# Optimization experiments

Measured on AMD Instinct MI355X. Metric: run time of the kernel, lower is better.

## Reference

```python
import jax, jax.numpy as jnp
import numpy as np

L, H, C, V, T_BLK = 12, 12, 768, 50257, 1024
D = C // H  # head dim = 64


def _layernorm(x, g, b, eps=1e-5):
    m = jnp.mean(x, axis=-1, keepdims=True)
    v = jnp.mean(jnp.square(x - m), axis=-1, keepdims=True)
    return (x - m) * jax.lax.rsqrt(v + eps) * g + b


def setup_inputs() -> dict:
    key = jax.random.key(0)
    ks = jax.random.split(key, 8)
    B, T = 8, 1024
    s = 0.02
    sp = 0.02 / np.sqrt(2 * L)  # c_proj special init
    return {
        "idx": jax.random.randint(ks[0], (B, T), 0, V, dtype=jnp.int32),
        "wte": jax.random.normal(ks[1], (V, C), jnp.float32) * s,
        "wpe": jax.random.normal(ks[2], (T_BLK, C), jnp.float32) * s,
        "ln1_g": jnp.ones((L, C), jnp.float32),
        "ln1_b": jnp.zeros((L, C), jnp.float32),
        "w_qkv": jax.random.normal(ks[3], (L, C, 3 * C), jnp.float32) * s,
        "b_qkv": jnp.zeros((L, 3 * C), jnp.float32),
        "w_ao": jax.random.normal(ks[4], (L, C, C), jnp.float32) * sp,
        "b_ao": jnp.zeros((L, C), jnp.float32),
        "ln2_g": jnp.ones((L, C), jnp.float32),
        "ln2_b": jnp.zeros((L, C), jnp.float32),
        "w_fc": jax.random.normal(ks[5], (L, C, 4 * C), jnp.float32) * s,
        "b_fc": jnp.zeros((L, 4 * C), jnp.float32),
        "w_mo": jax.random.normal(ks[6], (L, 4 * C, C), jnp.float32) * sp,
        "b_mo": jnp.zeros((L, C), jnp.float32),
        "lnf_g": jnp.ones((C,), jnp.float32),
        "lnf_b": jnp.zeros((C,), jnp.float32),
    }


def reference(idx, wte, wpe, ln1_g, ln1_b, w_qkv, b_qkv, w_ao, b_ao,
              ln2_g, ln2_b, w_fc, b_fc, w_mo, b_mo, lnf_g, lnf_b):
    B, T = idx.shape
    scale = 1.0 / np.sqrt(D)
    causal = jnp.tril(jnp.ones((T, T), dtype=bool))  # [T,T]

    x = wte[idx] + wpe[:T]  # [B,T,C]

    def block(x, p):
        g1, b1, wq, bq, wo, bo, g2, b2_, wf, bf, w2, b2m = p
        h = _layernorm(x, g1, b1)
        qkv = h @ wq + bq  # [B,T,3C]
        q, k, v = jnp.split(qkv, 3, axis=-1)
        q = q.reshape(B, T, H, D)
        k = k.reshape(B, T, H, D)
        v = v.reshape(B, T, H, D)
        att = jnp.einsum('bqhd,bkhd->bhqk', q, k) * scale
        att = jnp.where(causal, att, -jnp.inf)
        att = jax.nn.softmax(att, axis=-1)
        y = jnp.einsum('bhqk,bkhd->bqhd', att, v).reshape(B, T, C)
        x = x + y @ wo + bo
        h2 = _layernorm(x, g2, b2_)
        x = x + jax.nn.gelu(h2 @ wf + bf, approximate=False) @ w2 + b2m
        return x, None

    params = (ln1_g, ln1_b, w_qkv, b_qkv, w_ao, b_ao,
              ln2_g, ln2_b, w_fc, b_fc, w_mo, b_mo)
    x, _ = jax.lax.scan(block, x, params)

    x = _layernorm(x, lnf_g, lnf_b)
    # inference path: logits only for last position, lm_head tied to wte
    logits = x[:, -1:, :] @ wte.T  # [B,1,V]
    return logits
```

## Files before the change

### kernel.cpp

```cpp
#include <hip/hip_runtime.h>

#define B_ 8
#define T_ 1024
#define C_ 768
#define H_ 12
#define L_ 12
#define V_ 50257

typedef __bf16 bf16_t;
typedef __bf16 bf16x8 __attribute__((ext_vector_type(8)));
typedef __bf16 bf16x4 __attribute__((ext_vector_type(4)));
typedef float f32x4 __attribute__((ext_vector_type(4)));

__device__ __forceinline__ unsigned short f2bf(float f) {
  bf16_t h = (bf16_t)f;
  return __builtin_bit_cast(unsigned short, h);
}

__device__ __forceinline__ unsigned short bfbits(bf16_t h) {
  return __builtin_bit_cast(unsigned short, h);
}

template<int CTRL>
__device__ __forceinline__ float dppf(float x) {
  return __builtin_bit_cast(float, __builtin_amdgcn_update_dpp(
      0, __builtin_bit_cast(int, x), CTRL, 0xF, 0xF, true));
}
__device__ __forceinline__ float red16_max(float x) {
  x = fmaxf(x, dppf<0xB1>(x));
  x = fmaxf(x, dppf<0x4E>(x));
  x = fmaxf(x, dppf<0x124>(x));
  x = fmaxf(x, dppf<0x128>(x));
  return x;
}
__device__ __forceinline__ float red16_sum(float x) {
  x += dppf<0xB1>(x);
  x += dppf<0x4E>(x);
  x += dppf<0x124>(x);
  x += dppf<0x128>(x);
  return x;
}

__global__ __launch_bounds__(192) void embed_kernel(
    const int* __restrict__ idx, const float* __restrict__ wte,
    const float* __restrict__ wpe, float* __restrict__ xf)
{
  const int bt = blockIdx.x;
  const int t = bt & (T_ - 1);
  const int tok = idx[bt];
  const int c4 = threadIdx.x << 2;
  float4 a = *(const float4*)(wte + (size_t)tok * C_ + c4);
  float4 p = *(const float4*)(wpe + (size_t)t * C_ + c4);
  float4 r; r.x = a.x + p.x; r.y = a.y + p.y; r.z = a.z + p.z; r.w = a.w + p.w;
  *(float4*)(xf + (size_t)bt * C_ + c4) = r;
}

template<bool LAST>
__global__ __launch_bounds__(256) void ln_kernel(
    const float* __restrict__ x, const float* __restrict__ gw,
    const float* __restrict__ bw, unsigned short* __restrict__ obf,
    float* __restrict__ of)
{
  __shared__ float red[8];
  const size_t row = LAST ? ((size_t)blockIdx.x * T_ + (T_ - 1)) : (size_t)blockIdx.x;
  const float* xr = x + row * C_;
  const int t = threadIdx.x;
  float v0 = xr[t], v1 = xr[t + 256], v2 = xr[t + 512];
  float s = v0 + v1 + v2;
  #pragma unroll
  for (int off = 32; off; off >>= 1) s += __shfl_xor(s, off);
  if ((t & 63) == 0) red[t >> 6] = s;
  __syncthreads();
  const float mean = (red[0] + red[1] + red[2] + red[3]) * (1.0f / C_);
  const float d0 = v0 - mean, d1 = v1 - mean, d2 = v2 - mean;
  float ss = d0 * d0 + d1 * d1 + d2 * d2;
  #pragma unroll
  for (int off = 32; off; off >>= 1) ss += __shfl_xor(ss, off);
  if ((t & 63) == 0) red[4 + (t >> 6)] = ss;
  __syncthreads();
  const float var = (red[4] + red[5] + red[6] + red[7]) * (1.0f / C_);
  const float rs = rsqrtf(var + 1e-5f);
  float o0 = d0 * rs * gw[t] + bw[t];
  float o1 = d1 * rs * gw[t + 256] + bw[t + 256];
  float o2 = d2 * rs * gw[t + 512] + bw[t + 512];
  if (LAST) {
    float* orow = of + (size_t)blockIdx.x * C_;
    orow[t] = o0; orow[t + 256] = o1; orow[t + 512] = o2;
  } else {
    unsigned short* orow = obf + row * C_;
    orow[t] = f2bf(o0); orow[t + 256] = f2bf(o1); orow[t + 512] = f2bf(o2);
  }
}

__global__ __launch_bounds__(256) void cvtw4_kernel(
    const float* __restrict__ wq, const float* __restrict__ wa,
    const float* __restrict__ wf, const float* __restrict__ wm,
    unsigned short* __restrict__ out)
{
  __shared__ float tile[32][33];
  const int i = blockIdx.x;
  const float* W; unsigned short* Wt; int K, N, tix;
  if (i < 1728)      { W = wq; Wt = out;                 K = C_;     N = 3 * C_; tix = i; }
  else if (i < 2304) { W = wa; Wt = out + 3 * C_ * C_;   K = C_;     N = C_;     tix = i - 1728; }
  else if (i < 4608) { W = wf; Wt = out + 4 * C_ * C_;   K = C_;     N = 4 * C_; tix = i - 2304; }
  else               { W = wm; Wt = out + 8 * C_ * C_;   K = 4 * C_; N = C_;     tix = i - 4608; }
  const int ntx = N >> 5;
  const int kb = (tix / ntx) << 5, nb = (tix % ntx) << 5;
  const int t = threadIdx.x;
  {
    const int k = t >> 3, n4 = (t & 7) << 2;
    float4 v = *(const float4*)(W + (size_t)(kb + k) * N + nb + n4);
    tile[k][n4] = v.x; tile[k][n4 + 1] = v.y; tile[k][n4 + 2] = v.z; tile[k][n4 + 3] = v.w;
  }
  __syncthreads();
  {
    const int n = t >> 3, k4 = (t & 7) << 2;
    ushort4 o;
    o.x = f2bf(tile[k4][n]);     o.y = f2bf(tile[k4 + 1][n]);
    o.z = f2bf(tile[k4 + 2][n]); o.w = f2bf(tile[k4 + 3][n]);
    *(ushort4*)(Wt + (size_t)(nb + n) * K + kb + k4) = o;
  }
}

template<int EPI>
__global__ __launch_bounds__(256, 2) void gemm_bt(
    const unsigned short* __restrict__ A, const unsigned short* __restrict__ Bt,
    const float* __restrict__ bias, float* __restrict__ Cf,
    unsigned short* __restrict__ Cb, int M, int N, int K, int nx)
{
  __shared__ unsigned short As[2][128 * 64];
  __shared__ unsigned short Bs[2][128 * 64];
  const int tid = threadIdx.x;
  const int lane = tid & 63;
  const int w = tid >> 6;
  const int wr = w >> 1, wc = w & 1;
  const int l15 = lane & 15, l4 = lane >> 4;
  const int swz = lane & 7;

  const int nwg = gridDim.x;
  int wg = blockIdx.x;
  wg = (wg & 7) * (nwg >> 3) + (wg >> 3);
  const int mblk = wg / nx;
  const int nblk = wg - mblk * nx;
  const int m0 = mblk * 128, n0 = nblk * 128;

  f32x4 acc[4][4] = {};

  const int srow = lane >> 3;
  const int schunk = (lane & 7) ^ srow;
  const unsigned short* aSrc = A + (size_t)(m0 + w * 32 + srow) * K + schunk * 8;
  const unsigned short* bSrc = Bt + (size_t)(n0 + w * 32 + srow) * K + schunk * 8;
  const int ldsRowBase = (w * 32) * 64;

  auto stage = [&](int kt, int p) {
    const int k0 = kt << 6;
    #pragma unroll
    for (int j = 0; j < 4; ++j)
      __builtin_amdgcn_global_load_lds(
          (const __attribute__((address_space(1))) unsigned int*)(aSrc + (size_t)j * 8 * K + k0),
          (__attribute__((address_space(3))) unsigned int*)(&As[p][ldsRowBase + j * 8 * 64]), 16, 0, 0);
    #pragma unroll
    for (int j = 0; j < 4; ++j)
      __builtin_amdgcn_global_load_lds(
          (const __attribute__((address_space(1))) unsigned int*)(bSrc + (size_t)j * 8 * K + k0),
          (__attribute__((address_space(3))) unsigned int*)(&Bs[p][ldsRowBase + j * 8 * 64]), 16, 0, 0);
  };

  auto compute = [&](int p) {
    const unsigned short* aw = &As[p][(wr * 64) * 64];
    const unsigned short* bw2 = &Bs[p][(wc * 64) * 64];
    #pragma unroll
    for (int ks = 0; ks < 2; ++ks) {
      bf16x8 af[4], bf[4];
      #pragma unroll
      for (int mf = 0; mf < 4; ++mf)
        af[mf] = *(const bf16x8*)(aw + (mf * 16 + l15) * 64 + (((ks << 2) | l4) ^ swz) * 8);
      #pragma unroll
      for (int nf = 0; nf < 4; ++nf)
        bf[nf] = *(const bf16x8*)(bw2 + (nf * 16 + l15) * 64 + (((ks << 2) | l4) ^ swz) * 8);
      __builtin_amdgcn_s_setprio(1);
      #pragma unroll
      for (int mf = 0; mf < 4; ++mf)
        #pragma unroll
        for (int nf = 0; nf < 4; ++nf)
          acc[mf][nf] = __builtin_amdgcn_mfma_f32_16x16x32_bf16(af[mf], bf[nf], acc[mf][nf], 0, 0, 0);
      __builtin_amdgcn_s_setprio(0);
    }
  };

  const int nk = K >> 6;
  stage(0, 0);
  for (int kt = 0; kt < nk - 1; ++kt) {
    const int p = kt & 1;
    stage(kt + 1, p ^ 1);
    asm volatile("s_waitcnt vmcnt(8)" ::: "memory");
    __builtin_amdgcn_s_barrier();
    compute(p);
    __builtin_amdgcn_s_barrier();
  }
  asm volatile("s_waitcnt vmcnt(0)" ::: "memory");
  __builtin_amdgcn_s_barrier();
  compute((nk - 1) & 1);

  #pragma unroll
  for (int mf = 0; mf < 4; ++mf) {
    #pragma unroll
    for (int nf = 0; nf < 4; ++nf) {
      const int col = n0 + wc * 64 + nf * 16 + l15;
      const float bv = bias[col];
      int hh = 0, dd = 0;
      unsigned short* qkvo = nullptr;
      if constexpr (EPI == 3) {
        const int which = col / C_;
        const int rem = col - which * C_;
        hh = rem >> 6; dd = rem & 63;
        qkvo = Cb + (size_t)which * ((size_t)B_ * H_ * T_ * 64);
      }
      #pragma unroll
      for (int i = 0; i < 4; ++i) {
        const int row = m0 + wr * 64 + mf * 16 + l4 * 4 + i;
        float v = acc[mf][nf][i] + bv;
        if constexpr (EPI == 0) {
          Cf[(size_t)row * N + col] = v;
        } else if constexpr (EPI == 1) {
          Cf[(size_t)row * N + col] += v;
        } else if constexpr (EPI == 2) {
          float g = 0.5f * v * (1.0f + erff(v * 0.70710678118f));
          Cb[(size_t)row * N + col] = f2bf(g);
        } else {
          const int bb = row >> 10, tt = row & (T_ - 1);
          qkvo[(((size_t)bb * H_ + hh) * T_ + tt) * 64 + dd] = f2bf(v);
        }
      }
    }
  }
}

__global__ __launch_bounds__(256) void attn_kernel(
    const unsigned short* __restrict__ Qb, const unsigned short* __restrict__ Kb,
    const unsigned short* __restrict__ Vb, unsigned short* __restrict__ y)
{
  const int pb = blockIdx.x / 96;
  const int bh = blockIdx.x % 96;
  const int h = bh % H_;
  const int b = bh / H_;
  const int tid = threadIdx.x, lane = tid & 63, w = tid >> 6;
  const int l15 = lane & 15, l4 = lane >> 4;

  const int qw = (w < 2) ? (pb * 64 + w * 32) : ((15 - pb) * 64 + (w - 2) * 32);
  const int NT = (17 - pb) >> 1;

  __shared__ unsigned short Ks[128 * 64];
  __shared__ unsigned short Vt[64 * 136];
  __shared__ unsigned short Pb[4][32 * 74];

  const unsigned short* qp = Qb + ((size_t)bh * T_ + qw) * 64;
  bf16x8 qf[2][2];
  #pragma unroll
  for (int mf = 0; mf < 2; ++mf)
    #pragma unroll
    for (int ks = 0; ks < 2; ++ks)
      qf[mf][ks] = *(const bf16x8*)(qp + (mf * 16 + l15) * 64 + ks * 32 + l4 * 8);

  f32x4 o[2][4] = {};
  float mrow[2][4], lrow[2][4];
  #pragma unroll
  for (int mf = 0; mf < 2; ++mf)
    #pragma unroll
    for (int i = 0; i < 4; ++i) { mrow[mf][i] = -1e30f; lrow[mf][i] = 0.0f; }

  const unsigned short* kb0 = Kb + (size_t)bh * T_ * 64;
  const unsigned short* vb0 = Vb + (size_t)bh * T_ * 64;
  const int ck = w;
  const int skey = lane;
  const int sw = (skey & 7);

  bf16x8 kr0, kr1, kr2, kr3, vr0, vr1, vr2, vr3;
  {
    const unsigned short* kp = kb0 + (size_t)skey * 64;
    const unsigned short* vp = vb0 + (size_t)skey * 64;
    kr0 = *(const bf16x8*)(kp + ck * 8);
    kr1 = *(const bf16x8*)(kp + (ck + 4) * 8);
    kr2 = *(const bf16x8*)(kp + 64 * 64 + ck * 8);
    kr3 = *(const bf16x8*)(kp + 64 * 64 + (ck + 4) * 8);
    vr0 = *(const bf16x8*)(vp + ck * 8);
    vr1 = *(const bf16x8*)(vp + (ck + 4) * 8);
    vr2 = *(const bf16x8*)(vp + 64 * 64 + ck * 8);
    vr3 = *(const bf16x8*)(vp + 64 * 64 + (ck + 4) * 8);
  }

  for (int kt = 0; kt < NT; ++kt) {
    const int k0 = kt << 7;
    __syncthreads();
    *(bf16x8*)(Ks + skey * 64 + ((ck ^ sw) * 8)) = kr0;
    *(bf16x8*)(Ks + skey * 64 + (((ck + 4) ^ sw) * 8)) = kr1;
    *(bf16x8*)(Ks + (skey + 64) * 64 + ((ck ^ sw) * 8)) = kr2;
    *(bf16x8*)(Ks + (skey + 64) * 64 + (((ck + 4) ^ sw) * 8)) = kr3;
    #pragma unroll
    for (int j = 0; j < 8; ++j) {
      Vt[(ck * 8 + j) * 136 + skey]            = bfbits(vr0[j]);
      Vt[((ck + 4) * 8 + j) * 136 + skey]      = bfbits(vr1[j]);
      Vt[(ck * 8 + j) * 136 + skey + 64]       = bfbits(vr2[j]);
      Vt[((ck + 4) * 8 + j) * 136 + skey + 64] = bfbits(vr3[j]);
    }
    __syncthreads();
    if (kt + 1 < NT) {
      const int kn = (kt + 1) << 7;
      const unsigned short* kp = kb0 + (size_t)(kn + skey) * 64;
      const unsigned short* vp = vb0 + (size_t)(kn + skey) * 64;
      kr0 = *(const bf16x8*)(kp + ck * 8);
      kr1 = *(const bf16x8*)(kp + (ck + 4) * 8);
      kr2 = *(const bf16x8*)(kp + 64 * 64 + ck * 8);
      kr3 = *(const bf16x8*)(kp + 64 * 64 + (ck + 4) * 8);
      vr0 = *(const bf16x8*)(vp + ck * 8);
      vr1 = *(const bf16x8*)(vp + (ck + 4) * 8);
      vr2 = *(const bf16x8*)(vp + 64 * 64 + ck * 8);
      vr3 = *(const bf16x8*)(vp + 64 * 64 + (ck + 4) * 8);
    }

    #pragma unroll
    for (int h2 = 0; h2 < 2; ++h2) {
      const int kh0 = k0 + h2 * 64;
      if (kh0 > qw + 31) continue;

      f32x4 s[2][4] = {};
      __builtin_amdgcn_s_setprio(1);
      #pragma unroll
      for (int ks = 0; ks < 2; ++ks) {
        #pragma unroll
        for (int nfk = 0; nfk < 4; ++nfk) {
          const int key = h2 * 64 + nfk * 16 + l15;
          bf16x8 kf = *(const bf16x8*)(Ks + key * 64 + ((((ks << 2) | l4) ^ (l15 & 7)) * 8));
          #pragma unroll
          for (int mf = 0; mf < 2; ++mf)
            s[mf][nfk] = __builtin_amdgcn_mfma_f32_16x16x32_bf16(qf[mf][ks], kf, s[mf][nfk], 0, 0, 0);
        }
      }
      __builtin_amdgcn_s_setprio(0);

      #pragma unroll
      for (int mf = 0; mf < 2; ++mf) {
        const int qrow = qw + mf * 16 + l4 * 4;
        const bool fullt = (kh0 + 63) <= (qw + mf * 16);
        float alpha[4];
        float pvv[4][4];
        #pragma unroll
        for (int i = 0; i < 4; ++i) {
          const int q = qrow + i;
          float sv[4], tm = -1e30f;
          #pragma unroll
          for (int nfk = 0; nfk < 4; ++nfk) {
            float x = s[mf][nfk][i] * 0.125f;
            sv[nfk] = fullt ? x : ((kh0 + nfk * 16 + l15 <= q) ? x : -1e30f);
            tm = fmaxf(tm, sv[nfk]);
          }
          tm = red16_max(tm);
          const float mnew = fmaxf(mrow[mf][i], tm);
          alpha[i] = __expf(mrow[mf][i] - mnew);
          mrow[mf][i] = mnew;
          float rsum = 0.0f;
          #pragma unroll
          for (int nfk = 0; nfk < 4; ++nfk) {
            const float p = __expf(sv[nfk] - mnew);
            pvv[nfk][i] = p; rsum += p;
          }
          rsum = red16_sum(rsum);
          lrow[mf][i] = lrow[mf][i] * alpha[i] + rsum;
        }
        #pragma unroll
        for (int nf = 0; nf < 4; ++nf)
          #pragma unroll
          for (int i = 0; i < 4; ++i)
            o[mf][nf][i] *= alpha[i];
        #pragma unroll
        for (int nfk = 0; nfk < 4; ++nfk)
          #pragma unroll
          for (int i = 0; i < 4; ++i)
            Pb[w][(mf * 16 + l4 * 4 + i) * 74 + nfk * 16 + l15] = f2bf(pvv[nfk][i]);
      }

      bf16x8 pa[2][2];
      #pragma unroll
      for (int mf = 0; mf < 2; ++mf)
        #pragma unroll
        for (int k2 = 0; k2 < 2; ++k2)
          pa[mf][k2] = *(const bf16x8*)(Pb[w] + (mf * 16 + l15) * 74 + k2 * 32 + l4 * 8);
      __builtin_amdgcn_s_setprio(1);
      #pragma unroll
      for (int nf = 0; nf < 4; ++nf) {
        const int d = nf * 16 + l15;
        #pragma unroll
        for (int k2 = 0; k2 < 2; ++k2) {
          bf16x8 vf = *(const bf16x8*)(Vt + d * 136 + h2 * 64 + k2 * 32 + l4 * 8);
          #pragma unroll
          for (int mf = 0; mf < 2; ++mf)
            o[mf][nf] = __builtin_amdgcn_mfma_f32_16x16x32_bf16(pa[mf][k2], vf, o[mf][nf], 0, 0, 0);
        }
      }
      __builtin_amdgcn_s_setprio(0);
    }
  }

  #pragma unroll
  for (int mf = 0; mf < 2; ++mf) {
    #pragma unroll
    for (int i = 0; i < 4; ++i) {
      const float inv = 1.0f / lrow[mf][i];
      const int q = qw + mf * 16 + l4 * 4 + i;
      unsigned short* yr = y + (size_t)(b * T_ + q) * C_ + h * 64;
      #pragma unroll
      for (int nf = 0; nf < 4; ++nf)
        yr[nf * 16 + l15] = f2bf(o[mf][nf][i] * inv);
    }
  }
}

__global__ __launch_bounds__(256) void head_kernel(
    const float* __restrict__ lnf, const float* __restrict__ wte,
    float* __restrict__ out)
{
  __shared__ float xs[B_ * C_];
  for (int i = threadIdx.x; i < B_ * C_; i += 256) xs[i] = lnf[i];
  __syncthreads();
  const int w = threadIdx.x >> 6, lane = threadIdx.x & 63;
  const int v = blockIdx.x * 4 + w;
  if (v >= V_) return;
  const float* wv = wte + (size_t)v * C_ + lane * 12;
  float4 w0 = *(const float4*)(wv);
  float4 w1 = *(const float4*)(wv + 4);
  float4 w2 = *(const float4*)(wv + 8);
  float acc[B_];
  #pragma unroll
  for (int bb = 0; bb < B_; ++bb) {
    const float* xr = xs + bb * C_ + lane * 12;
    float4 x0 = *(const float4*)(xr);
    float4 x1 = *(const float4*)(xr + 4);
    float4 x2 = *(const float4*)(xr + 8);
    acc[bb] = w0.x * x0.x + w0.y * x0.y + w0.z * x0.z + w0.w * x0.w
            + w1.x * x1.x + w1.y * x1.y + w1.z * x1.z + w1.w * x1.w
            + w2.x * x2.x + w2.y * x2.y + w2.z * x2.z + w2.w * x2.w;
  }
  #pragma unroll
  for (int off = 32; off; off >>= 1) {
    #pragma unroll
    for (int bb = 0; bb < B_; ++bb)
      acc[bb] += __shfl_xor(acc[bb], off);
  }
  if (lane == 0) {
    #pragma unroll
    for (int bb = 0; bb < B_; ++bb)
      out[(size_t)bb * V_ + v] = acc[bb];
  }
}

extern "C" void kernel_launch(void* const* d_in, const int* in_sizes, int n_in,
                              void* d_out, int out_size, void* d_ws, size_t ws_size,
                              hipStream_t stream)
{
  (void)in_sizes; (void)n_in; (void)out_size; (void)ws_size;
  const int*   idx   = (const int*)d_in[0];
  const float* wte   = (const float*)d_in[1];
  const float* wpe   = (const float*)d_in[2];
  const float* ln1_g = (const float*)d_in[3];
  const float* ln1_b = (const float*)d_in[4];
  const float* w_qkv = (const float*)d_in[5];
  const float* b_qkv = (const float*)d_in[6];
  const float* w_ao  = (const float*)d_in[7];
  const float* b_ao  = (const float*)d_in[8];
  const float* ln2_g = (const float*)d_in[9];
  const float* ln2_b = (const float*)d_in[10];
  const float* w_fc  = (const float*)d_in[11];
  const float* b_fc  = (const float*)d_in[12];
  const float* w_mo  = (const float*)d_in[13];
  const float* b_mo  = (const float*)d_in[14];
  const float* lnf_g = (const float*)d_in[15];
  const float* lnf_b = (const float*)d_in[16];

  char* ws = (char*)d_ws;
  size_t off = 0;
  auto wsalloc = [&](size_t bytes) -> void* {
    void* p = ws + off;
    off += (bytes + 255) & ~(size_t)255;
    return p;
  };
  const size_t SZH = (size_t)B_ * H_ * T_ * 64;
  float* xf             = (float*)wsalloc((size_t)B_ * T_ * C_ * 4);
  unsigned short* qkv3  = (unsigned short*)wsalloc(3 * SZH * 2);
  unsigned short* a_in  = (unsigned short*)wsalloc((size_t)B_ * T_ * C_ * 2);
  unsigned short* act2  = (unsigned short*)wsalloc((size_t)B_ * T_ * 4 * C_ * 2);
  unsigned short* wbuf  = (unsigned short*)wsalloc((size_t)12 * C_ * C_ * 2);
  float* lnfb           = (float*)wsalloc((size_t)B_ * C_ * 4);

  const size_t OFF_AO = (size_t)3 * C_ * C_;
  const size_t OFF_FC = (size_t)4 * C_ * C_;
  const size_t OFF_MO = (size_t)8 * C_ * C_;
  const int MROWS = B_ * T_;

  embed_kernel<<<B_ * T_, 192, 0, stream>>>(idx, wte, wpe, xf);

  for (int l = 0; l < L_; ++l) {
    ln_kernel<false><<<B_ * T_, 256, 0, stream>>>(xf, ln1_g + l * C_, ln1_b + l * C_, a_in, nullptr);
    cvtw4_kernel<<<6912, 256, 0, stream>>>(
        w_qkv + (size_t)l * C_ * 3 * C_, w_ao + (size_t)l * C_ * C_,
        w_fc + (size_t)l * C_ * 4 * C_, w_mo + (size_t)l * 4 * C_ * C_, wbuf);
    gemm_bt<3><<<18 * 64, 256, 0, stream>>>(a_in, wbuf, b_qkv + l * 3 * C_, nullptr, qkv3, MROWS, 3 * C_, C_, 18);
    attn_kernel<<<8 * B_ * H_, 256, 0, stream>>>(qkv3, qkv3 + SZH, qkv3 + 2 * SZH, a_in);
    gemm_bt<1><<<6 * 64, 256, 0, stream>>>(a_in, wbuf + OFF_AO, b_ao + l * C_, xf, nullptr, MROWS, C_, C_, 6);
    ln_kernel<false><<<B_ * T_, 256, 0, stream>>>(xf, ln2_g + l * C_, ln2_b + l * C_, a_in, nullptr);
    gemm_bt<2><<<24 * 64, 256, 0, stream>>>(a_in, wbuf + OFF_FC, b_fc + l * 4 * C_, nullptr, act2, MROWS, 4 * C_, C_, 24);
    gemm_bt<1><<<6 * 64, 256, 0, stream>>>(act2, wbuf + OFF_MO, b_mo + l * C_, xf, nullptr, MROWS, C_, 4 * C_, 6);
  }

  ln_kernel<true><<<B_, 256, 0, stream>>>(xf, lnf_g, lnf_b, nullptr, lnfb);
  head_kernel<<<(V_ + 3) / 4, 256, 0, stream>>>(lnfb, wte, (float*)d_out);
}
```

Measured before the change: 3.742 ms.

## Replace GEMM with 8-wave 256x128 tile kernel and interleaved fragment loads

Swaps the 4-wave 128x128 GEMM for a 512-thread kernel computing 256x128 tiles. Each wave owns a 64x64 sub-tile, and the kernel splits the MFMA work into four quadrants separated by barriers, with LDS fragment loads interleaved between them. The aim is more operand reuse per loaded B tile and overlap of LDS reads with matrix math. In exchange, the grid is halved: the 768-wide GEMMs launch only 192 workgroups, which may underfill the device, and the added barriers cost synchronisation.

```diff
diff --git a/kernel.cpp b/kernel.cpp
--- a/kernel.cpp
+++ b/kernel.cpp
@@ -11,6 +11,9 @@
 typedef __bf16 bf16x8 __attribute__((ext_vector_type(8)));
 typedef __bf16 bf16x4 __attribute__((ext_vector_type(4)));
 typedef float f32x4 __attribute__((ext_vector_type(4)));
+
+#define AS1 __attribute__((address_space(1)))
+#define AS3 __attribute__((address_space(3)))
 
 __device__ __forceinline__ unsigned short f2bf(float f) {
   bf16_t h = (bf16_t)f;
@@ -123,84 +126,126 @@
 }
 
 template<int EPI>
-__global__ __launch_bounds__(256, 2) void gemm_bt(
+__global__ __launch_bounds__(512, 1) void gemm8(
     const unsigned short* __restrict__ A, const unsigned short* __restrict__ Bt,
     const float* __restrict__ bias, float* __restrict__ Cf,
     unsigned short* __restrict__ Cb, int M, int N, int K, int nx)
 {
-  __shared__ unsigned short As[2][128 * 64];
-  __shared__ unsigned short Bs[2][128 * 64];
+  __shared__ __align__(16) unsigned short As[2][2][128 * 64];
+  __shared__ __align__(16) unsigned short Bs[2][128 * 64];
   const int tid = threadIdx.x;
   const int lane = tid & 63;
   const int w = tid >> 6;
-  const int wr = w >> 1, wc = w & 1;
+  const int wr = w >> 1;
+  const int wc = w & 1;
   const int l15 = lane & 15, l4 = lane >> 4;
-  const int swz = lane & 7;
+  const int s7 = l15 & 7;
+  const int hA = wr >> 1;
+  const int rbase = (wr & 1) * 64;
 
   const int nwg = gridDim.x;
   int wg = blockIdx.x;
   wg = (wg & 7) * (nwg >> 3) + (wg >> 3);
   const int mblk = wg / nx;
   const int nblk = wg - mblk * nx;
-  const int m0 = mblk * 128, n0 = nblk * 128;
+  const int m0 = mblk * 256, n0 = nblk * 128;
 
   f32x4 acc[4][4] = {};
 
-  const int srow = lane >> 3;
-  const int schunk = (lane & 7) ^ srow;
-  const unsigned short* aSrc = A + (size_t)(m0 + w * 32 + srow) * K + schunk * 8;
-  const unsigned short* bSrc = Bt + (size_t)(n0 + w * 32 + srow) * K + schunk * 8;
-  const int ldsRowBase = (w * 32) * 64;
+  const int srow8 = lane >> 3;
+  const int schunk = (lane & 7) ^ srow8;
+  const unsigned short* aS00 = A  + (size_t)(m0 +       0 + w * 8 + srow8) * K + schunk * 8;
+  const unsigned short* aS01 = A  + (size_t)(m0 +      64 + w * 8 + srow8) * K + schunk * 8;
+  const unsigned short* aS10 = A  + (size_t)(m0 + 128 + 0 + w * 8 + srow8) * K + schunk * 8;
+  const unsigned short* aS11 = A  + (size_t)(m0 + 128 + 64 + w * 8 + srow8) * K + schunk * 8;
+  const unsigned short* bS0  = Bt + (size_t)(n0 +       0 + w * 8 + srow8) * K + schunk * 8;
+  const unsigned short* bS1  = Bt + (size_t)(n0 +      64 + w * 8 + srow8) * K + schunk * 8;
+  const int ldsw0 = (0 * 8 + w) * 512;
+  const int ldsw1 = (1 * 8 + w) * 512;
 
   auto stage = [&](int kt, int p) {
-    const int k0 = kt << 6;
-    #pragma unroll
-    for (int j = 0; j < 4; ++j)
-      __builtin_amdgcn_global_load_lds(
-          (const __attribute__((address_space(1))) unsigned int*)(aSrc + (size_t)j * 8 * K + k0),
-          (__attribute__((address_space(3))) unsigned int*)(&As[p][ldsRowBase + j * 8 * 64]), 16, 0, 0);
-    #pragma unroll
-    for (int j = 0; j < 4; ++j)
-      __builtin_amdgcn_global_load_lds(
-          (const __attribute__((address_space(1))) unsigned int*)(bSrc + (size_t)j * 8 * K + k0),
-          (__attribute__((address_space(3))) unsigned int*)(&Bs[p][ldsRowBase + j * 8 * 64]), 16, 0, 0);
-  };
-
-  auto compute = [&](int p) {
-    const unsigned short* aw = &As[p][(wr * 64) * 64];
-    const unsigned short* bw2 = &Bs[p][(wc * 64) * 64];
-    #pragma unroll
-    for (int ks = 0; ks < 2; ++ks) {
-      bf16x8 af[4], bf[4];
-      #pragma unroll
-      for (int mf = 0; mf < 4; ++mf)
-        af[mf] = *(const bf16x8*)(aw + (mf * 16 + l15) * 64 + (((ks << 2) | l4) ^ swz) * 8);
-      #pragma unroll
-      for (int nf = 0; nf < 4; ++nf)
-        bf[nf] = *(const bf16x8*)(bw2 + (nf * 16 + l15) * 64 + (((ks << 2) | l4) ^ swz) * 8);
-      __builtin_amdgcn_s_setprio(1);
-      #pragma unroll
-      for (int mf = 0; mf < 4; ++mf)
-        #pragma unroll
-        for (int nf = 0; nf < 4; ++nf)
-          acc[mf][nf] = __builtin_amdgcn_mfma_f32_16x16x32_bf16(af[mf], bf[nf], acc[mf][nf], 0, 0, 0);
-      __builtin_amdgcn_s_setprio(0);
-    }
+    const size_t k0 = (size_t)kt * 64;
+    __builtin_amdgcn_global_load_lds((const AS1 unsigned int*)(aS00 + k0), (AS3 unsigned int*)(&As[p][0][ldsw0]), 16, 0, 0);
+    __builtin_amdgcn_global_load_lds((const AS1 unsigned int*)(aS01 + k0), (AS3 unsigned int*)(&As[p][0][ldsw1]), 16, 0, 0);
+    __builtin_amdgcn_global_load_lds((const AS1 unsigned int*)(aS10 + k0), (AS3 unsigned int*)(&As[p][1][ldsw0]), 16, 0, 0);
+    __builtin_amdgcn_global_load_lds((const AS1 unsigned int*)(aS11 + k0), (AS3 unsigned int*)(&As[p][1][ldsw1]), 16, 0, 0);
+    __builtin_amdgcn_global_load_lds((const AS1 unsigned int*)(bS0  + k0), (AS3 unsigned int*)(&Bs[p][ldsw0]), 16, 0, 0);
+    __builtin_amdgcn_global_load_lds((const AS1 unsigned int*)(bS1  + k0), (AS3 unsigned int*)(&Bs[p][ldsw1]), 16, 0, 0);
   };
 
   const int nk = K >> 6;
   stage(0, 0);
-  for (int kt = 0; kt < nk - 1; ++kt) {
-    const int p = kt & 1;
-    stage(kt + 1, p ^ 1);
-    asm volatile("s_waitcnt vmcnt(8)" ::: "memory");
+
+  for (int t = 0; t < nk; ++t) {
+    const int p = t & 1;
+    bf16x8 af[4][2], bf[4][2];
+    auto rdA = [&](int mf, int ks) -> bf16x8 {
+      return *(const bf16x8*)(&As[p][hA][(rbase + mf * 16 + l15) * 64 + ((((ks << 2) | l4) ^ s7) << 3)]);
+    };
+    auto rdB = [&](int nf, int ks) -> bf16x8 {
+      return *(const bf16x8*)(&Bs[p][(wc * 64 + nf * 16 + l15) * 64 + ((((ks << 2) | l4) ^ s7) << 3)]);
+    };
+
+    if (t + 1 < nk) {
+      stage(t + 1, p ^ 1);
+      asm volatile("s_waitcnt vmcnt(6)" ::: "memory");
+    } else {
+      asm volatile("s_waitcnt vmcnt(0)" ::: "memory");
+    }
     __builtin_amdgcn_s_barrier();
-    compute(p);
+    #pragma unroll
+    for (int mf = 0; mf < 2; ++mf) { af[mf][0] = rdA(mf, 0); af[mf][1] = rdA(mf, 1); }
+    #pragma unroll
+    for (int nf = 0; nf < 2; ++nf) { bf[nf][0] = rdB(nf, 0); bf[nf][1] = rdB(nf, 1); }
+    __builtin_amdgcn_s_setprio(1);
+    #pragma unroll
+    for (int mf = 0; mf < 2; ++mf)
+      #pragma unroll
+      for (int nf = 0; nf < 2; ++nf)
+        #pragma unroll
+        for (int ks = 0; ks < 2; ++ks)
+          acc[mf][nf] = __builtin_amdgcn_mfma_f32_16x16x32_bf16(af[mf][ks], bf[nf][ks], acc[mf][nf], 0, 0, 0);
+    __builtin_amdgcn_s_setprio(0);
     __builtin_amdgcn_s_barrier();
-  }
-  asm volatile("s_waitcnt vmcnt(0)" ::: "memory");
-  __builtin_amdgcn_s_barrier();
-  compute((nk - 1) & 1);
+
+    #pragma unroll
+    for (int nf = 2; nf < 4; ++nf) { bf[nf][0] = rdB(nf, 0); bf[nf][1] = rdB(nf, 1); }
+    __builtin_amdgcn_s_barrier();
+    __builtin_amdgcn_s_setprio(1);
+    #pragma unroll
+    for (int mf = 0; mf < 2; ++mf)
+      #pragma unroll
+      for (int nf = 2; nf < 4; ++nf)
+        #pragma unroll
+        for (int ks = 0; ks < 2; ++ks)
+          acc[mf][nf] = __builtin_amdgcn_mfma_f32_16x16x32_bf16(af[mf][ks], bf[nf][ks], acc[mf][nf], 0, 0, 0);
+    __builtin_amdgcn_s_setprio(0);
+    __builtin_amdgcn_s_barrier();
+
+    #pragma unroll
+    for (int mf = 2; mf < 4; ++mf) { af[mf][0] = rdA(mf, 0); af[mf][1] = rdA(mf, 1); }
+    __builtin_amdgcn_s_barrier();
+    __builtin_amdgcn_s_setprio(1);
+    #pragma unroll
+    for (int mf = 2; mf < 4; ++mf)
+      #pragma unroll
+      for (int nf = 0; nf < 2; ++nf)
+        #pragma unroll
+        for (int ks = 0; ks < 2; ++ks)
+          acc[mf][nf] = __builtin_amdgcn_mfma_f32_16x16x32_bf16(af[mf][ks], bf[nf][ks], acc[mf][nf], 0, 0, 0);
+    __builtin_amdgcn_s_setprio(0);
+    __builtin_amdgcn_s_barrier();
+
+    __builtin_amdgcn_s_setprio(1);
+    #pragma unroll
+    for (int mf = 2; mf < 4; ++mf)
+      #pragma unroll
+      for (int nf = 2; nf < 4; ++nf)
+        #pragma unroll
+        for (int ks = 0; ks < 2; ++ks)
+          acc[mf][nf] = __builtin_amdgcn_mfma_f32_16x16x32_bf16(af[mf][ks], bf[nf][ks], acc[mf][nf], 0, 0, 0);
+    __builtin_amdgcn_s_setprio(0);
+  }
 
   #pragma unroll
   for (int mf = 0; mf < 4; ++mf) {
@@ -220,9 +265,7 @@
       for (int i = 0; i < 4; ++i) {
         const int row = m0 + wr * 64 + mf * 16 + l4 * 4 + i;
         float v = acc[mf][nf][i] + bv;
-        if constexpr (EPI == 0) {
-          Cf[(size_t)row * N + col] = v;
-        } else if constexpr (EPI == 1) {
+        if constexpr (EPI == 1) {
           Cf[(size_t)row * N + col] += v;
         } else if constexpr (EPI == 2) {
           float g = 0.5f * v * (1.0f + erff(v * 0.70710678118f));
@@ -503,12 +546,12 @@
     cvtw4_kernel<<<6912, 256, 0, stream>>>(
         w_qkv + (size_t)l * C_ * 3 * C_, w_ao + (size_t)l * C_ * C_,
         w_fc + (size_t)l * C_ * 4 * C_, w_mo + (size_t)l * 4 * C_ * C_, wbuf);
-    gemm_bt<3><<<18 * 64, 256, 0, stream>>>(a_in, wbuf, b_qkv + l * 3 * C_, nullptr, qkv3, MROWS, 3 * C_, C_, 18);
+    gemm8<3><<<32 * 18, 512, 0, stream>>>(a_in, wbuf, b_qkv + l * 3 * C_, nullptr, qkv3, MROWS, 3 * C_, C_, 18);
     attn_kernel<<<8 * B_ * H_, 256, 0, stream>>>(qkv3, qkv3 + SZH, qkv3 + 2 * SZH, a_in);
-    gemm_bt<1><<<6 * 64, 256, 0, stream>>>(a_in, wbuf + OFF_AO, b_ao + l * C_, xf, nullptr, MROWS, C_, C_, 6);
+    gemm8<1><<<32 * 6, 512, 0, stream>>>(a_in, wbuf + OFF_AO, b_ao + l * C_, xf, nullptr, MROWS, C_, C_, 6);
     ln_kernel<false><<<B_ * T_, 256, 0, stream>>>(xf, ln2_g + l * C_, ln2_b + l * C_, a_in, nullptr);
-    gemm_bt<2><<<24 * 64, 256, 0, stream>>>(a_in, wbuf + OFF_FC, b_fc + l * 4 * C_, nullptr, act2, MROWS, 4 * C_, C_, 24);
-    gemm_bt<1><<<6 * 64, 256, 0, stream>>>(act2, wbuf + OFF_MO, b_mo + l * C_, xf, nullptr, MROWS, C_, 4 * C_, 6);
+    gemm8<2><<<32 * 24, 512, 0, stream>>>(a_in, wbuf + OFF_FC, b_fc + l * 4 * C_, nullptr, act2, MROWS, 4 * C_, C_, 24);
+    gemm8<1><<<32 * 6, 512, 0, stream>>>(act2, wbuf + OFF_MO, b_mo + l * C_, xf, nullptr, MROWS, C_, 4 * C_, 6);
   }
 
   ln_kernel<true><<<B_, 256, 0, stream>>>(xf, lnf_g, lnf_b, nullptr, lnfb);
```

New measurement: 4.198 ms. 12.2% more time.

## Remap GEMM tiles per XCD and lazily rescale attention softmax max

Applied to the files above, without the earlier changes.

The GEMM block index mapping now gives each XCD a contiguous group of 8 M-blocks and walks N-blocks across the blocks of that XCD. The aim is for weight and activation tiles to be reused in each XCD's L2. The attention online softmax now rescales the accumulator and row sum only when some row's new max exceeds the stored max by more than 8, which is checked wave-wide with __any. This skips most exp and multiply rescale work, at the cost of probabilities that can grow up to e^8 before rescaling, which is safe in fp32 but may lose a little bf16 precision in P.

```diff
diff --git a/kernel.cpp b/kernel.cpp
--- a/kernel.cpp
+++ b/kernel.cpp
@@ -11,6 +11,9 @@
 typedef __bf16 bf16x8 __attribute__((ext_vector_type(8)));
 typedef __bf16 bf16x4 __attribute__((ext_vector_type(4)));
 typedef float f32x4 __attribute__((ext_vector_type(4)));
+
+#define AS1 __attribute__((address_space(1)))
+#define AS3 __attribute__((address_space(3)))
 
 __device__ __forceinline__ unsigned short f2bf(float f) {
   bf16_t h = (bf16_t)f;
@@ -128,6 +131,7 @@
     const float* __restrict__ bias, float* __restrict__ Cf,
     unsigned short* __restrict__ Cb, int M, int N, int K, int nx)
 {
+  (void)M; (void)nx;
   __shared__ unsigned short As[2][128 * 64];
   __shared__ unsigned short Bs[2][128 * 64];
   const int tid = threadIdx.x;
@@ -137,11 +141,11 @@
   const int l15 = lane & 15, l4 = lane >> 4;
   const int swz = lane & 7;
 
-  const int nwg = gridDim.x;
-  int wg = blockIdx.x;
-  wg = (wg & 7) * (nwg >> 3) + (wg >> 3);
-  const int mblk = wg / nx;
-  const int nblk = wg - mblk * nx;
+  const int bid = blockIdx.x;
+  const int xcd = bid & 7;
+  const int j = bid >> 3;
+  const int mblk = xcd * 8 + (j & 7);
+  const int nblk = j >> 3;
   const int m0 = mblk * 128, n0 = nblk * 128;
 
   f32x4 acc[4][4] = {};
@@ -155,15 +159,15 @@
   auto stage = [&](int kt, int p) {
     const int k0 = kt << 6;
     #pragma unroll
-    for (int j = 0; j < 4; ++j)
+    for (int jj = 0; jj < 4; ++jj)
       __builtin_amdgcn_global_load_lds(
-          (const __attribute__((address_space(1))) unsigned int*)(aSrc + (size_t)j * 8 * K + k0),
-          (__attribute__((address_space(3))) unsigned int*)(&As[p][ldsRowBase + j * 8 * 64]), 16, 0, 0);
-    #pragma unroll
-    for (int j = 0; j < 4; ++j)
+          (const AS1 unsigned int*)(aSrc + (size_t)jj * 8 * K + k0),
+          (AS3 unsigned int*)(&As[p][ldsRowBase + jj * 8 * 64]), 16, 0, 0);
+    #pragma unroll
+    for (int jj = 0; jj < 4; ++jj)
       __builtin_amdgcn_global_load_lds(
-          (const __attribute__((address_space(1))) unsigned int*)(bSrc + (size_t)j * 8 * K + k0),
-          (__attribute__((address_space(3))) unsigned int*)(&Bs[p][ldsRowBase + j * 8 * 64]), 16, 0, 0);
+          (const AS1 unsigned int*)(bSrc + (size_t)jj * 8 * K + k0),
+          (AS3 unsigned int*)(&Bs[p][ldsRowBase + jj * 8 * 64]), 16, 0, 0);
   };
 
   auto compute = [&](int p) {
@@ -220,9 +224,7 @@
       for (int i = 0; i < 4; ++i) {
         const int row = m0 + wr * 64 + mf * 16 + l4 * 4 + i;
         float v = acc[mf][nf][i] + bv;
-        if constexpr (EPI == 0) {
-          Cf[(size_t)row * N + col] = v;
-        } else if constexpr (EPI == 1) {
+        if constexpr (EPI == 1) {
           Cf[(size_t)row * N + col] += v;
         } else if constexpr (EPI == 2) {
           float g = 0.5f * v * (1.0f + erff(v * 0.70710678118f));
@@ -297,11 +299,11 @@
     *(bf16x8*)(Ks + (skey + 64) * 64 + ((ck ^ sw) * 8)) = kr2;
     *(bf16x8*)(Ks + (skey + 64) * 64 + (((ck + 4) ^ sw) * 8)) = kr3;
     #pragma unroll
-    for (int j = 0; j < 8; ++j) {
-      Vt[(ck * 8 + j) * 136 + skey]            = bfbits(vr0[j]);
-      Vt[((ck + 4) * 8 + j) * 136 + skey]      = bfbits(vr1[j]);
-      Vt[(ck * 8 + j) * 136 + skey + 64]       = bfbits(vr2[j]);
-      Vt[((ck + 4) * 8 + j) * 136 + skey + 64] = bfbits(vr3[j]);
+    for (int jj = 0; jj < 8; ++jj) {
+      Vt[(ck * 8 + jj) * 136 + skey]            = bfbits(vr0[jj]);
+      Vt[((ck + 4) * 8 + jj) * 136 + skey]      = bfbits(vr1[jj]);
+      Vt[(ck * 8 + jj) * 136 + skey + 64]       = bfbits(vr2[jj]);
+      Vt[((ck + 4) * 8 + jj) * 136 + skey + 64] = bfbits(vr3[jj]);
     }
     __syncthreads();
     if (kt + 1 < NT) {
@@ -342,36 +344,45 @@
       for (int mf = 0; mf < 2; ++mf) {
         const int qrow = qw + mf * 16 + l4 * 4;
         const bool fullt = (kh0 + 63) <= (qw + mf * 16);
-        float alpha[4];
-        float pvv[4][4];
+        float pvv[4][4], tm[4];
         #pragma unroll
         for (int i = 0; i < 4; ++i) {
           const int q = qrow + i;
-          float sv[4], tm = -1e30f;
+          float m_ = -1e30f;
           #pragma unroll
           for (int nfk = 0; nfk < 4; ++nfk) {
             float x = s[mf][nfk][i] * 0.125f;
-            sv[nfk] = fullt ? x : ((kh0 + nfk * 16 + l15 <= q) ? x : -1e30f);
-            tm = fmaxf(tm, sv[nfk]);
+            x = fullt ? x : ((kh0 + nfk * 16 + l15 <= q) ? x : -1e30f);
+            pvv[nfk][i] = x;
+            m_ = fmaxf(m_, x);
           }
-          tm = red16_max(tm);
-          const float mnew = fmaxf(mrow[mf][i], tm);
-          alpha[i] = __expf(mrow[mf][i] - mnew);
-          mrow[mf][i] = mnew;
+          tm[i] = red16_max(m_);
+        }
+        bool need = false;
+        #pragma unroll
+        for (int i = 0; i < 4; ++i) need |= (tm[i] > mrow[mf][i] + 8.0f);
+        if (__any(need)) {
+          #pragma unroll
+          for (int i = 0; i < 4; ++i) {
+            const float mnew = fmaxf(mrow[mf][i], tm[i]);
+            const float alpha = __expf(mrow[mf][i] - mnew);
+            mrow[mf][i] = mnew;
+            lrow[mf][i] *= alpha;
+            #pragma unroll
+            for (int nf = 0; nf < 4; ++nf) o[mf][nf][i] *= alpha;
+          }
+        }
+        #pragma unroll
+        for (int i = 0; i < 4; ++i) {
           float rsum = 0.0f;
           #pragma unroll
           for (int nfk = 0; nfk < 4; ++nfk) {
-            const float p = __expf(sv[nfk] - mnew);
+            const float p = __expf(pvv[nfk][i] - mrow[mf][i]);
             pvv[nfk][i] = p; rsum += p;
           }
           rsum = red16_sum(rsum);
-          lrow[mf][i] = lrow[mf][i] * alpha[i] + rsum;
+          lrow[mf][i] += rsum;
         }
-        #pragma unroll
-        for (int nf = 0; nf < 4; ++nf)
-          #pragma unroll
-          for (int i = 0; i < 4; ++i)
-            o[mf][nf][i] *= alpha[i];
         #pragma unroll
         for (int nfk = 0; nfk < 4; ++nfk)
           #pragma unroll
@@ -503,12 +514,12 @@
     cvtw4_kernel<<<6912, 256, 0, stream>>>(
         w_qkv + (size_t)l * C_ * 3 * C_, w_ao + (size_t)l * C_ * C_,
         w_fc + (size_t)l * C_ * 4 * C_, w_mo + (size_t)l * 4 * C_ * C_, wbuf);
-    gemm_bt<3><<<18 * 64, 256, 0, stream>>>(a_in, wbuf, b_qkv + l * 3 * C_, nullptr, qkv3, MROWS, 3 * C_, C_, 18);
+    gemm_bt<3><<<64 * 18, 256, 0, stream>>>(a_in, wbuf, b_qkv + l * 3 * C_, nullptr, qkv3, MROWS, 3 * C_, C_, 18);
     attn_kernel<<<8 * B_ * H_, 256, 0, stream>>>(qkv3, qkv3 + SZH, qkv3 + 2 * SZH, a_in);
-    gemm_bt<1><<<6 * 64, 256, 0, stream>>>(a_in, wbuf + OFF_AO, b_ao + l * C_, xf, nullptr, MROWS, C_, C_, 6);
+    gemm_bt<1><<<64 * 6, 256, 0, stream>>>(a_in, wbuf + OFF_AO, b_ao + l * C_, xf, nullptr, MROWS, C_, C_, 6);
     ln_kernel<false><<<B_ * T_, 256, 0, stream>>>(xf, ln2_g + l * C_, ln2_b + l * C_, a_in, nullptr);
-    gemm_bt<2><<<24 * 64, 256, 0, stream>>>(a_in, wbuf + OFF_FC, b_fc + l * 4 * C_, nullptr, act2, MROWS, 4 * C_, C_, 24);
-    gemm_bt<1><<<6 * 64, 256, 0, stream>>>(act2, wbuf + OFF_MO, b_mo + l * C_, xf, nullptr, MROWS, C_, 4 * C_, 6);
+    gemm_bt<2><<<64 * 24, 256, 0, stream>>>(a_in, wbuf + OFF_FC, b_fc + l * 4 * C_, nullptr, act2, MROWS, 4 * C_, C_, 24);
+    gemm_bt<1><<<64 * 6, 256, 0, stream>>>(act2, wbuf + OFF_MO, b_mo + l * C_, xf, nullptr, MROWS, C_, 4 * C_, 6);
   }
 
   ln_kernel<true><<<B_, 256, 0, stream>>>(xf, lnf_g, lnf_b, nullptr, lnfb);
```

Result: no change. 3.713 ms (-0.8%).
